# Optimization experiments

Hardware: AMD Instinct MI355X
Metric: run time of the kernel (lower is better)

## Reference

```python
import jax, jax.numpy as jnp
import numpy as np
import math

B, S, H, DM = 1, 2048, 16, 1024
DK = DM // H
MAX_SEQ = 2048  # rel_embed has MAX_SEQ+1 rows


def setup_inputs() -> dict:
    rng = jax.random.key(0)
    ks = jax.random.split(rng, 12)
    w = lambda k, shape, s=0.02: (jax.random.normal(k, shape, jnp.float32) * s)
    inp = {
        'query': jax.random.normal(ks[0], (B, S, DM), jnp.float32),
        'key':   jax.random.normal(ks[1], (B, S, DM), jnp.float32),
        'value': jax.random.normal(ks[2], (B, S, DM), jnp.float32),
        # causal integer mask [B,S,S] (cumsum over it derives rel-pos indices)
        'mask': jnp.broadcast_to(jnp.tril(jnp.ones((S, S), jnp.int32)), (B, S, S)),
        'Wq': w(ks[3], (DM, DM)), 'bq': jnp.zeros((DM,), jnp.float32),
        'Wk': w(ks[4], (DM, DM)), 'bk': jnp.zeros((DM,), jnp.float32),
        'Wv': w(ks[5], (DM, DM)), 'bv': jnp.zeros((DM,), jnp.float32),
        'Wo': w(ks[6], (DM, DM)), 'bo': jnp.zeros((DM,), jnp.float32),
        # relative position embeddings [h, max_seq_len+1, d_k], N(0,1) as in the module
        'rel_embed': jax.random.normal(ks[7], (H, MAX_SEQ + 1, DK), jnp.float32),
    }
    return inp


def reference(query, key, value, mask, Wq, bq, Wk, bk, Wv, bv, Wo, bo, rel_embed):
    scale = 1.0 / math.sqrt(DK)
    heads = lambda x, W, b: (x @ W.T + b).reshape(B, S, H, DK).transpose(0, 2, 1, 3)
    q = heads(query, Wq, bq)   # [B,H,S,DK]
    k = heads(key, Wk, bk)
    v = heads(value, Wv, bv)

    scores = jnp.einsum('bhid,bhjd->bhij', q, k) * scale  # [B,H,S,S]

    m4 = mask[:, None, :, :]                 # [B,1,S,S]
    nz = m4 != 0
    # torch: cumsum(mask)-1 picks the m-index; index 0 (then zeroed) where mask==0
    m_idx = jnp.where(nz, jnp.cumsum(m4, axis=-1) - 1, 0)  # [B,1,S,S]

    # rel_scores[b,h,m,l] = <q[b,h,l,:], rel_embed[h,m,:]> / sqrt(d_k)
    rel = jnp.einsum('bhld,hmd->bhml', q, rel_embed[:, :S]) * scale  # [B,H,S,S]
    idx = jnp.broadcast_to(m_idx, (B, H, S, S))
    # torch.take flat-index decodes to rel[b,h, m_idx[i,j], j]
    rel_g = jnp.take_along_axis(rel, idx, axis=2) * nz.astype(scores.dtype)

    scores = jnp.where(nz, scores + rel_g, jnp.float32(-1e9))
    p = jax.nn.softmax(scores, axis=-1)      # dropout p=0.0 -> identity

    out = jnp.einsum('bhij,bhjd->bhid', p, v)         # [B,H,S,DK]
    out = out.transpose(0, 2, 1, 3).reshape(B, S, DM)  # [B,S,DM]
    return out @ Wo.T + bo
```

## Files before the change

kernel.cpp:

```cpp
#include <hip/hip_runtime.h>

typedef __bf16 bf16_t;
typedef __bf16 bf16x4 __attribute__((ext_vector_type(4)));
typedef __bf16 bf16x8 __attribute__((ext_vector_type(8)));
typedef float  f32x4  __attribute__((ext_vector_type(4)));
typedef float  f32x16 __attribute__((ext_vector_type(16)));
typedef unsigned int u32;

#define S_LEN 2048
#define DMODEL 1024
#define NHEAD 16
#define DHEAD 64
#define RELROWS 2049

__device__ __forceinline__ void gload16(const void* g, void* l) {
    __builtin_amdgcn_global_load_lds((const __attribute__((address_space(1))) void*)g,
                                     (__attribute__((address_space(3))) void*)l,
                                     16, 0, 0);
}

__device__ __forceinline__ f32x4 mfma16(bf16x8 a, bf16x8 b, f32x4 c) {
    return __builtin_amdgcn_mfma_f32_16x16x32_bf16(a, b, c, 0, 0, 0);
}
__device__ __forceinline__ f32x16 mfma32(bf16x8 a, bf16x8 b, f32x16 c) {
    return __builtin_amdgcn_mfma_f32_32x32x16_bf16(a, b, c, 0, 0, 0);
}

__device__ __forceinline__ bf16x8 lds_read_swz(const bf16_t* base, int row, int colb) {
    return *(const bf16x8*)((const char*)base + row * 128 + (colb ^ ((row & 7) << 4)));
}

__device__ __forceinline__ u32 cvtpk(float lo, float hi) {
    u32 w;
    asm("v_cvt_pk_bf16_f32 %0, %1, %2" : "=v"(w) : "v"(lo), "v"(hi));
    return w;
}
__device__ __forceinline__ void swap32(u32& a, u32& b) {
    asm("v_permlane32_swap_b32 %0, %1" : "+v"(a), "+v"(b));
}
__device__ __forceinline__ float fexp2(float x) {
    float r;
    asm("v_exp_f32 %0, %1" : "=v"(r) : "v"(x));
    return r;
}

__global__ __launch_bounds__(256)
void f2bf_all(const float* __restrict__ xq, const float* __restrict__ xk,
              const float* __restrict__ xv,
              const float* __restrict__ wq, const float* __restrict__ wk,
              const float* __restrict__ wv, const float* __restrict__ wo,
              bf16_t* __restrict__ dst, int n4X, int n4W) {
    const int i = blockIdx.x * blockDim.x + threadIdx.x;
    const float* src; int j;
    if (i < 3 * n4X) {
        if (i < n4X)            { src = xq; j = i; }
        else if (i < 2 * n4X)   { src = xk; j = i - n4X; }
        else                    { src = xv; j = i - 2 * n4X; }
    } else {
        int w = i - 3 * n4X;
        if (w < n4W)            { src = wq; j = w; }
        else if (w < 2 * n4W)   { src = wk; j = w - n4W; }
        else if (w < 3 * n4W)   { src = wv; j = w - 2 * n4W; }
        else                    { src = wo; j = w - 3 * n4W; }
    }
    float4 v = ((const float4*)src)[j];
    bf16x4 o;
    o[0] = (bf16_t)v.x; o[1] = (bf16_t)v.y; o[2] = (bf16_t)v.z; o[3] = (bf16_t)v.w;
    ((bf16x4*)dst)[i] = o;
}

template <int BM, int BN>
__global__ __launch_bounds__(256)
void gemm_qkv(const bf16_t* __restrict__ Abase, const bf16_t* __restrict__ Wbase,
              const float* __restrict__ b0, const float* __restrict__ b1,
              const float* __restrict__ b2,
              bf16_t* __restrict__ outb,
              const float* __restrict__ relp, float* __restrict__ RGout,
              bf16_t* __restrict__ vtp,
              int M, int N, int K) {
    __shared__ alignas(16) bf16_t As[2][BM * 64];
    __shared__ alignas(16) bf16_t Bs[2][BN * 64];
    const int tid = threadIdx.x, lane = tid & 63, wave = tid >> 6;
    const int z = blockIdx.z;
    const bf16_t* A = Abase + (size_t)z * M * K;
    const bf16_t* W = Wbase + (size_t)z * N * K;
    const float* bias = (z == 0) ? b0 : (z == 1 ? b1 : b2);
    const int nwg = gridDim.x * gridDim.y;
    const int wg = blockIdx.y * gridDim.x + blockIdx.x;
    const int swz = (wg & 7) * (nwg >> 3) + (wg >> 3);
    const int m0 = (swz / gridDim.x) * BM, n0 = (swz % gridDim.x) * BN;
    const int wr = (wave >> 1) * (BM / 2), wc = (wave & 1) * (BN / 2);
    constexpr int MR = BM / 32, NR = BN / 32;
    constexpr int LOADS = BM / 32 + BN / 32;

    f32x4 acc[MR][NR] = {};
    const int soff = wave * 1024 + lane * 16;

    auto stage = [&](int b, int kt) {
#pragma unroll
        for (int r = 0; r < BM / 32; ++r) {
            int L = r * 4096 + soff;
            int row = L >> 7, colb = (L & 127) ^ ((row & 7) << 4);
            gload16(A + (size_t)(m0 + row) * K + kt + (colb >> 1),
                    (char*)As[b] + r * 4096 + wave * 1024);
        }
#pragma unroll
        for (int r = 0; r < BN / 32; ++r) {
            int L = r * 4096 + soff;
            int row = L >> 7, colb = (L & 127) ^ ((row & 7) << 4);
            gload16(W + (size_t)(n0 + row) * K + kt + (colb >> 1),
                    (char*)Bs[b] + r * 4096 + wave * 1024);
        }
    };

    const int NK = K >> 6;
    stage(0, 0);
    for (int s = 0; s < NK; ++s) {
        const int buf = s & 1;
        if (s + 1 < NK) {
            stage(buf ^ 1, (s + 1) << 6);
            if constexpr (LOADS == 6) asm volatile("s_waitcnt vmcnt(6)" ::: "memory");
            else if constexpr (LOADS == 4) asm volatile("s_waitcnt vmcnt(4)" ::: "memory");
            else asm volatile("s_waitcnt vmcnt(8)" ::: "memory");
        } else {
            asm volatile("s_waitcnt vmcnt(0)" ::: "memory");
        }
        asm volatile("s_barrier" ::: "memory");
#pragma unroll
        for (int kk = 0; kk < 2; ++kk) {
            bf16x8 af[MR], bfr[NR];
#pragma unroll
            for (int m = 0; m < MR; ++m)
                af[m] = lds_read_swz(As[buf], wr + m * 16 + (lane & 15),
                                     kk * 64 + (lane >> 4) * 16);
#pragma unroll
            for (int n = 0; n < NR; ++n)
                bfr[n] = lds_read_swz(Bs[buf], wc + n * 16 + (lane & 15),
                                      kk * 64 + (lane >> 4) * 16);
#pragma unroll
            for (int m = 0; m < MR; ++m)
#pragma unroll
                for (int n = 0; n < NR; ++n)
                    acc[m][n] = mfma16(af[m], bfr[n], acc[m][n]);
        }
        asm volatile("s_barrier" ::: "memory");
    }

    const float scale = (z == 0) ? 0.18033688011112042f : 1.0f;
    float rp[MR][4];
#pragma unroll
    for (int m = 0; m < MR; ++m)
#pragma unroll
        for (int r2 = 0; r2 < 4; ++r2) rp[m][r2] = 0.f;
    const int hh = n0 >> 6;
#pragma unroll
    for (int m = 0; m < MR; ++m) {
        const int gi = m0 + wr + m * 16 + (lane >> 4) * 4;
#pragma unroll
        for (int n = 0; n < NR; ++n) {
            const int gj = n0 + wc + n * 16 + (lane & 15);
            const float bv = bias[gj];
            if (z == 2) {
                bf16x4 o4;
#pragma unroll
                for (int r2 = 0; r2 < 4; ++r2) o4[r2] = (bf16_t)(acc[m][n][r2] + bv);
                *(bf16x4*)&vtp[(size_t)gj * S_LEN + gi] = o4;
            } else {
#pragma unroll
                for (int r2 = 0; r2 < 4; ++r2) {
                    float v = (acc[m][n][r2] + bv) * scale;
                    outb[(size_t)z * M * N + (size_t)(gi + r2) * N + gj] = (bf16_t)v;
                    if (z == 0)
                        rp[m][r2] += v * relp[((size_t)hh * RELROWS + (gi + r2)) * DHEAD + (gj & 63)];
                }
            }
        }
    }
    if (z == 0) {
        constexpr int HM = BM / 2;
        float* Rp = (float*)As;
#pragma unroll
        for (int m = 0; m < MR; ++m)
#pragma unroll
            for (int r2 = 0; r2 < 4; ++r2) {
                float p = rp[m][r2];
                p += __shfl_xor(p, 1);
                p += __shfl_xor(p, 2);
                p += __shfl_xor(p, 4);
                p += __shfl_xor(p, 8);
                if ((lane & 15) == 0)
                    Rp[wave * HM + m * 16 + (lane >> 4) * 4 + r2] = p;
            }
        __syncthreads();
        if ((wave & 1) == 0) {
#pragma unroll
            for (int rr0 = 0; rr0 < HM; rr0 += 64) {
                int rr = rr0 + lane;
                float v = Rp[wave * HM + rr] + Rp[(wave + 1) * HM + rr];
                RGout[hh * S_LEN + m0 + wr + rr] = v;
            }
        }
    }
}

__global__ __launch_bounds__(512)
void gemm_out(const bf16_t* __restrict__ A, const bf16_t* __restrict__ W,
              const float* __restrict__ bias, float* __restrict__ outf,
              int M, int N, int K) {
    __shared__ alignas(16) bf16_t As[2][2][64 * 64];
    __shared__ alignas(16) bf16_t Bs[2][2][64 * 64];
    const int tid = threadIdx.x, lane = tid & 63, wave = tid >> 6;
    const int grp = wave >> 2, w4 = wave & 3;
    const int nwg = gridDim.x * gridDim.y;
    const int wg = blockIdx.y * gridDim.x + blockIdx.x;
    const int swz = (wg & 7) * (nwg >> 3) + (wg >> 3);
    const int m0 = (swz / gridDim.x) * 64, n0 = (swz % gridDim.x) * 64;
    const int wr = (w4 >> 1) * 32, wc = (w4 & 1) * 32;
    const int kbase = grp * (K >> 1);

    f32x4 acc[2][2] = {};
    const int soff = w4 * 1024 + lane * 16;

    auto stage = [&](int b, int kt) {
#pragma unroll
        for (int r = 0; r < 2; ++r) {
            int L = r * 4096 + soff;
            int row = L >> 7, colb = (L & 127) ^ ((row & 7) << 4);
            gload16(A + (size_t)(m0 + row) * K + kt + (colb >> 1),
                    (char*)As[grp][b] + r * 4096 + w4 * 1024);
            gload16(W + (size_t)(n0 + row) * K + kt + (colb >> 1),
                    (char*)Bs[grp][b] + r * 4096 + w4 * 1024);
        }
    };

    const int NKg = K >> 7;
    stage(0, kbase);
    for (int s = 0; s < NKg; ++s) {
        const int buf = s & 1;
        if (s + 1 < NKg) {
            stage(buf ^ 1, kbase + ((s + 1) << 6));
            asm volatile("s_waitcnt vmcnt(4)" ::: "memory");
        } else {
            asm volatile("s_waitcnt vmcnt(0)" ::: "memory");
        }
        asm volatile("s_barrier" ::: "memory");
#pragma unroll
        for (int kk = 0; kk < 2; ++kk) {
            bf16x8 af[2], bfr[2];
#pragma unroll
            for (int m = 0; m < 2; ++m)
                af[m] = lds_read_swz(As[grp][buf], wr + m * 16 + (lane & 15),
                                     kk * 64 + (lane >> 4) * 16);
#pragma unroll
            for (int n = 0; n < 2; ++n)
                bfr[n] = lds_read_swz(Bs[grp][buf], wc + n * 16 + (lane & 15),
                                      kk * 64 + (lane >> 4) * 16);
#pragma unroll
            for (int m = 0; m < 2; ++m)
#pragma unroll
                for (int n = 0; n < 2; ++n)
                    acc[m][n] = mfma16(af[m], bfr[n], acc[m][n]);
        }
        asm volatile("s_barrier" ::: "memory");
    }

    float* scr = (float*)As;
    if (grp == 1) {
        float* base = scr + ((w4 * 64 + lane) << 4);
#pragma unroll
        for (int m = 0; m < 2; ++m)
#pragma unroll
            for (int n = 0; n < 2; ++n)
                *(f32x4*)(base + (m * 2 + n) * 4) = acc[m][n];
    }
    __syncthreads();
    if (grp == 0) {
        const float* base = scr + ((w4 * 64 + lane) << 4);
#pragma unroll
        for (int m = 0; m < 2; ++m) {
            const int gi = m0 + wr + m * 16 + (lane >> 4) * 4;
#pragma unroll
            for (int n = 0; n < 2; ++n) {
                f32x4 ov = *(const f32x4*)(base + (m * 2 + n) * 4);
                const int gj = n0 + wc + n * 16 + (lane & 15);
                const float bv = bias[gj];
#pragma unroll
                for (int r2 = 0; r2 < 4; ++r2)
                    outf[(size_t)(gi + r2) * N + gj] = acc[m][n][r2] + ov[r2] + bv;
            }
        }
    }
}

__global__ __launch_bounds__(256, 2)
void flash_attn(const bf16_t* __restrict__ Qb, const bf16_t* __restrict__ Kb,
                const bf16_t* __restrict__ Vtp, const float* __restrict__ RG,
                bf16_t* __restrict__ Ob) {
    __shared__ alignas(16) bf16_t KB[4][64 * 64];
    __shared__ alignas(16) bf16_t VB[4][64 * 64];
    __shared__ alignas(16) float Rs[S_LEN];
    const int tid = threadIdx.x, lane = tid & 63, wave = tid >> 6;
    const int h = blockIdx.x;
    const int qt = (int)gridDim.y - 1 - (int)blockIdx.y;
    const int q0 = qt * 32;
    const int nt = (qt >> 1) + 1;
    const int qpar = qt & 1;
    const int lo5 = lane & 31, hi = lane >> 5;

    const int nkv = nt * 64;
    for (int i = tid * 8; i < nkv; i += 2048) {
        *(float4*)&Rs[i]     = *(const float4*)&RG[h * S_LEN + i];
        *(float4*)&Rs[i + 4] = *(const float4*)&RG[h * S_LEN + i + 4];
    }

    const bf16_t* qp = Qb + (size_t)(q0 + lo5) * DMODEL + h * DHEAD;
    bf16x8 qf[4];
#pragma unroll
    for (int c = 0; c < 4; ++c)
        qf[c] = *(const bf16x8*)(qp + c * 16 + hi * 8);

    auto stageK = [&](int tt) {
        char* dst = (char*)KB[wave];
#pragma unroll
        for (int rr = 0; rr < 8; ++rr) {
            int L = rr * 1024 + lane * 16;
            int row = L >> 7, colb = (L & 127) ^ ((row & 7) << 4);
            gload16(Kb + (size_t)(tt * 64 + row) * DMODEL + h * DHEAD + (colb >> 1),
                    dst + rr * 1024);
        }
    };
    auto stageV = [&](int tt) {
        char* dst = (char*)VB[wave];
#pragma unroll
        for (int rr = 0; rr < 8; ++rr) {
            int L = rr * 1024 + lane * 16;
            int row = L >> 7, colb = (L & 127) ^ ((row & 7) << 4);
            gload16(Vtp + (size_t)(h * DHEAD + row) * S_LEN + tt * 64 + (colb >> 1),
                    dst + rr * 1024);
        }
    };

    if (wave < nt) { stageK(wave); stageV(wave); }
    __syncthreads();

    f32x16 oacc[2] = {};
    float ls = 0.f;
    const int thr = qpar * 32 + lo5;

    for (int tt = wave; tt < nt; tt += 4) {
        const int kv0 = tt * 64;
        const bool diag = (tt == nt - 1);
        asm volatile("s_waitcnt vmcnt(8)" ::: "memory");

        f32x16 sta, stb;
#pragma unroll
        for (int g = 0; g < 4; ++g) {
            f32x4 ra = *(const f32x4*)&Rs[kv0 + g * 8 + hi * 4];
            f32x4 rb = *(const f32x4*)&Rs[kv0 + 32 + g * 8 + hi * 4];
#pragma unroll
            for (int e = 0; e < 4; ++e) { sta[g * 4 + e] = ra[e]; stb[g * 4 + e] = rb[e]; }
        }
        __builtin_amdgcn_s_setprio(1);
#pragma unroll
        for (int c = 0; c < 4; ++c) {
            bf16x8 kfa = lds_read_swz(KB[wave], lo5, c * 32 + hi * 16);
            sta = mfma32(kfa, qf[c], sta);
        }
#pragma unroll
        for (int c = 0; c < 4; ++c) {
            bf16x8 kfb = lds_read_swz(KB[wave], 32 + lo5, c * 32 + hi * 16);
            stb = mfma32(kfb, qf[c], stb);
        }
        __builtin_amdgcn_s_setprio(0);
        if (tt + 4 < nt) stageK(tt + 4);

        float pra[16], prb[16];
        if (diag) {
#pragma unroll
            for (int r = 0; r < 16; ++r) {
                int kloc = (r & 3) + 8 * (r >> 2) + 4 * hi;
                float va = fexp2(sta[r]), vb = fexp2(stb[r]);
                pra[r] = (kloc > thr) ? 0.f : va;
                prb[r] = (kloc + 32 > thr) ? 0.f : vb;
            }
        } else {
#pragma unroll
            for (int r = 0; r < 16; ++r) { pra[r] = fexp2(sta[r]); prb[r] = fexp2(stb[r]); }
        }
#pragma unroll
        for (int r = 0; r < 16; ++r) ls += pra[r] + prb[r];
        u32 pw[4][4];
#pragma unroll
        for (int hf = 0; hf < 2; ++hf) {
            u32 a  = cvtpk(pra[8 * hf + 0], pra[8 * hf + 1]);
            u32 b  = cvtpk(pra[8 * hf + 4], pra[8 * hf + 5]);
            swap32(a, b);
            u32 c2 = cvtpk(pra[8 * hf + 2], pra[8 * hf + 3]);
            u32 d2 = cvtpk(pra[8 * hf + 6], pra[8 * hf + 7]);
            swap32(c2, d2);
            pw[hf][0] = a;  pw[hf][1] = c2;  pw[hf][2] = b;  pw[hf][3] = d2;
        }
#pragma unroll
        for (int hf = 0; hf < 2; ++hf) {
            u32 a  = cvtpk(prb[8 * hf + 0], prb[8 * hf + 1]);
            u32 b  = cvtpk(prb[8 * hf + 4], prb[8 * hf + 5]);
            swap32(a, b);
            u32 c2 = cvtpk(prb[8 * hf + 2], prb[8 * hf + 3]);
            u32 d2 = cvtpk(prb[8 * hf + 6], prb[8 * hf + 7]);
            swap32(c2, d2);
            pw[2 + hf][0] = a;  pw[2 + hf][1] = c2;  pw[2 + hf][2] = b;  pw[2 + hf][3] = d2;
        }

        if (tt + 4 < nt) asm volatile("s_waitcnt vmcnt(8)" ::: "memory");
        else             asm volatile("s_waitcnt vmcnt(0)" ::: "memory");

        __builtin_amdgcn_s_setprio(1);
#pragma unroll
        for (int kc = 0; kc < 4; ++kc) {
            union { u32 w[4]; bf16x8 v; } uu;
            uu.w[0] = pw[kc][0]; uu.w[1] = pw[kc][1]; uu.w[2] = pw[kc][2]; uu.w[3] = pw[kc][3];
#pragma unroll
            for (int db = 0; db < 2; ++db) {
                bf16x8 vf = lds_read_swz(VB[wave], db * 32 + lo5, kc * 32 + hi * 16);
                oacc[db] = mfma32(vf, uu.v, oacc[db]);
            }
        }
        __builtin_amdgcn_s_setprio(0);
        if (tt + 4 < nt) stageV(tt + 4);
    }

    asm volatile("s_waitcnt vmcnt(0)" ::: "memory");
    __syncthreads();
    float* scr = (float*)KB;
    if (wave > 0) {
        float* base = scr + (wave - 1) * 2112 + lane * 32;
#pragma unroll
        for (int db = 0; db < 2; ++db)
#pragma unroll
            for (int g = 0; g < 4; ++g) {
                f32x4 v4;
#pragma unroll
                for (int e = 0; e < 4; ++e) v4[e] = oacc[db][g * 4 + e];
                *(f32x4*)(base + db * 16 + g * 4) = v4;
            }
        scr[(wave - 1) * 2112 + 2048 + lane] = ls;
    }
    __syncthreads();
    if (wave == 0) {
#pragma unroll
        for (int w2 = 0; w2 < 3; ++w2) {
            const float* base = scr + w2 * 2112 + lane * 32;
#pragma unroll
            for (int db = 0; db < 2; ++db)
#pragma unroll
                for (int g = 0; g < 4; ++g) {
                    f32x4 v4 = *(const f32x4*)(base + db * 16 + g * 4);
#pragma unroll
                    for (int e = 0; e < 4; ++e) oacc[db][g * 4 + e] += v4[e];
                }
            ls += scr[w2 * 2112 + 2048 + lane];
        }
        ls += __shfl_xor(ls, 32);
        const float inv = 1.0f / ls;
        const int qg = q0 + lo5;
#pragma unroll
        for (int db = 0; db < 2; ++db)
#pragma unroll
            for (int g = 0; g < 4; ++g) {
                bf16x4 o4;
#pragma unroll
                for (int e = 0; e < 4; ++e)
                    o4[e] = (bf16_t)(oacc[db][g * 4 + e] * inv);
                *(bf16x4*)&Ob[(size_t)qg * DMODEL + h * DHEAD + db * 32 + g * 8 + hi * 4] = o4;
            }
    }
}

extern "C" void kernel_launch(void* const* d_in, const int* in_sizes, int n_in,
                              void* d_out, int out_size, void* d_ws, size_t ws_size,
                              hipStream_t stream) {
    const float* query = (const float*)d_in[0];
    const float* key   = (const float*)d_in[1];
    const float* value = (const float*)d_in[2];
    const float* Wq  = (const float*)d_in[4];
    const float* bq  = (const float*)d_in[5];
    const float* Wk  = (const float*)d_in[6];
    const float* bk  = (const float*)d_in[7];
    const float* Wv  = (const float*)d_in[8];
    const float* bv  = (const float*)d_in[9];
    const float* Wo  = (const float*)d_in[10];
    const float* bo  = (const float*)d_in[11];
    const float* rel = (const float*)d_in[12];

    char* ws = (char*)d_ws;
    const size_t nX = (size_t)S_LEN * DMODEL;
    const size_t nW = (size_t)DMODEL * DMODEL;
    bf16_t* Xbf  = (bf16_t*)ws;
    bf16_t* Wbf  = (bf16_t*)(ws + 3 * nX * 2);
    bf16_t* QKV  = (bf16_t*)(ws + 3 * nX * 2 + 4 * nW * 2);
    float*  RG   = (float*)(ws + 3 * nX * 2 + 4 * nW * 2 + 3 * nX * 2);
    bf16_t* Vtp  = QKV + 2 * nX;
    bf16_t* AOb  = (bf16_t*)(ws + nX * 2);
    (void)in_sizes; (void)n_in; (void)out_size; (void)ws_size;

    const int n4X = (int)(nX / 4), n4W = (int)(nW / 4);
    const int tot4 = 3 * n4X + 4 * n4W;
    f2bf_all<<<tot4 / 256, 256, 0, stream>>>(query, key, value, Wq, Wk, Wv, Wo,
                                             Xbf, n4X, n4W);

    gemm_qkv<128, 64><<<dim3(DMODEL / 64, S_LEN / 128, 3), 256, 0, stream>>>(
        Xbf, Wbf, bq, bk, bv, QKV, rel, RG, Vtp, S_LEN, DMODEL, DMODEL);

    flash_attn<<<dim3(NHEAD, S_LEN / 32), 256, 0, stream>>>(QKV, QKV + nX, Vtp, RG, AOb);

    gemm_out<<<dim3(DMODEL / 64, S_LEN / 64), 512, 0, stream>>>(
        AOb, Wbf + 3 * nW, bo, (float*)d_out, S_LEN, DMODEL, DMODEL);
}
```

Measured before the change: 79.46 us.

## Use 4-stage K=32 LDS pipeline with single barrier in QKV GEMM

The QKV projection GEMM main loop switches from a double-buffered K=64 tile to a four-buffer ring of K=32 tiles. Loads run three stages ahead and each iteration needs only one barrier, with a new 64-byte-row swizzle. MFMA issue is also raised in priority with s_setprio. The stage loader now hardcodes 2 A loads and 1 B load per wave, which implicitly assumes BM=128 and BN=64. Any other instantiation would load incorrectly, and the vmcnt constants assume 3 loads per stage.

```diff
diff --git a/kernel.cpp b/kernel.cpp
--- a/kernel.cpp
+++ b/kernel.cpp
@@ -28,6 +28,9 @@
 
 __device__ __forceinline__ bf16x8 lds_read_swz(const bf16_t* base, int row, int colb) {
     return *(const bf16x8*)((const char*)base + row * 128 + (colb ^ ((row & 7) << 4)));
+}
+__device__ __forceinline__ bf16x8 lds_read_swz32(const bf16_t* base, int row, int colb) {
+    return *(const bf16x8*)((const char*)base + row * 64 + (colb ^ (((row >> 1) & 3) << 4)));
 }
 
 __device__ __forceinline__ u32 cvtpk(float lo, float hi) {
@@ -78,8 +81,8 @@
               const float* __restrict__ relp, float* __restrict__ RGout,
               bf16_t* __restrict__ vtp,
               int M, int N, int K) {
-    __shared__ alignas(16) bf16_t As[2][BM * 64];
-    __shared__ alignas(16) bf16_t Bs[2][BN * 64];
+    __shared__ alignas(16) bf16_t As[4][BM * 32];
+    __shared__ alignas(16) bf16_t Bs[4][BN * 32];
     const int tid = threadIdx.x, lane = tid & 63, wave = tid >> 6;
     const int z = blockIdx.z;
     const bf16_t* A = Abase + (size_t)z * M * K;
@@ -91,59 +94,52 @@
     const int m0 = (swz / gridDim.x) * BM, n0 = (swz % gridDim.x) * BN;
     const int wr = (wave >> 1) * (BM / 2), wc = (wave & 1) * (BN / 2);
     constexpr int MR = BM / 32, NR = BN / 32;
-    constexpr int LOADS = BM / 32 + BN / 32;
 
     f32x4 acc[MR][NR] = {};
-    const int soff = wave * 1024 + lane * 16;
 
     auto stage = [&](int b, int kt) {
 #pragma unroll
-        for (int r = 0; r < BM / 32; ++r) {
-            int L = r * 4096 + soff;
-            int row = L >> 7, colb = (L & 127) ^ ((row & 7) << 4);
+        for (int r = 0; r < 2; ++r) {
+            int rr = wave * 2 + r;
+            int L = rr * 1024 + lane * 16;
+            int row = L >> 6;
+            int colb = (L & 63) ^ (((row >> 1) & 3) << 4);
             gload16(A + (size_t)(m0 + row) * K + kt + (colb >> 1),
-                    (char*)As[b] + r * 4096 + wave * 1024);
-        }
-#pragma unroll
-        for (int r = 0; r < BN / 32; ++r) {
-            int L = r * 4096 + soff;
-            int row = L >> 7, colb = (L & 127) ^ ((row & 7) << 4);
+                    (char*)As[b] + rr * 1024);
+        }
+        {
+            int rr = wave;
+            int L = rr * 1024 + lane * 16;
+            int row = L >> 6;
+            int colb = (L & 63) ^ (((row >> 1) & 3) << 4);
             gload16(W + (size_t)(n0 + row) * K + kt + (colb >> 1),
-                    (char*)Bs[b] + r * 4096 + wave * 1024);
+                    (char*)Bs[b] + rr * 1024);
         }
     };
 
-    const int NK = K >> 6;
-    stage(0, 0);
-    for (int s = 0; s < NK; ++s) {
-        const int buf = s & 1;
-        if (s + 1 < NK) {
-            stage(buf ^ 1, (s + 1) << 6);
-            if constexpr (LOADS == 6) asm volatile("s_waitcnt vmcnt(6)" ::: "memory");
-            else if constexpr (LOADS == 4) asm volatile("s_waitcnt vmcnt(4)" ::: "memory");
-            else asm volatile("s_waitcnt vmcnt(8)" ::: "memory");
-        } else {
-            asm volatile("s_waitcnt vmcnt(0)" ::: "memory");
-        }
+    const int NH = K >> 5;
+    stage(0, 0); stage(1, 32); stage(2, 64);
+    for (int s = 0; s < NH; ++s) {
+        if (s + 2 < NH)      asm volatile("s_waitcnt vmcnt(6)" ::: "memory");
+        else if (s + 1 < NH) asm volatile("s_waitcnt vmcnt(3)" ::: "memory");
+        else                 asm volatile("s_waitcnt vmcnt(0)" ::: "memory");
         asm volatile("s_barrier" ::: "memory");
-#pragma unroll
-        for (int kk = 0; kk < 2; ++kk) {
-            bf16x8 af[MR], bfr[NR];
-#pragma unroll
-            for (int m = 0; m < MR; ++m)
-                af[m] = lds_read_swz(As[buf], wr + m * 16 + (lane & 15),
-                                     kk * 64 + (lane >> 4) * 16);
+        if (s + 3 < NH) stage((s + 3) & 3, (s + 3) << 5);
+        const int buf = s & 3;
+        bf16x8 af[MR], bfr[NR];
+#pragma unroll
+        for (int m = 0; m < MR; ++m)
+            af[m] = lds_read_swz32(As[buf], wr + m * 16 + (lane & 15), (lane >> 4) * 16);
+#pragma unroll
+        for (int n = 0; n < NR; ++n)
+            bfr[n] = lds_read_swz32(Bs[buf], wc + n * 16 + (lane & 15), (lane >> 4) * 16);
+        __builtin_amdgcn_s_setprio(1);
+#pragma unroll
+        for (int m = 0; m < MR; ++m)
 #pragma unroll
             for (int n = 0; n < NR; ++n)
-                bfr[n] = lds_read_swz(Bs[buf], wc + n * 16 + (lane & 15),
-                                      kk * 64 + (lane >> 4) * 16);
-#pragma unroll
-            for (int m = 0; m < MR; ++m)
-#pragma unroll
-                for (int n = 0; n < NR; ++n)
-                    acc[m][n] = mfma16(af[m], bfr[n], acc[m][n]);
-        }
-        asm volatile("s_barrier" ::: "memory");
+                acc[m][n] = mfma16(af[m], bfr[n], acc[m][n]);
+        __builtin_amdgcn_s_setprio(0);
     }
 
     const float scale = (z == 0) ? 0.18033688011112042f : 1.0f;
```

New measurement: 85.46 us. +7.6%, slower.
